# Kernel tuning notes

Measured on AMD Instinct MI355X. Metric: run time of the kernel, lower is better.

The kernel has to match this reference:

```python
import jax, jax.numpy as jnp
import numpy as np

N = 50000       # nodes
E = 800000      # edges (before self-loops)
IN_DIM = 128
HID = 64
HEADS = 4
C = HID // HEADS  # 16 per-head channels
NEG_SLOPE = 0.2   # PyG GATConv default
BN_EPS = 1e-5


def setup_inputs() -> dict:
    key = jax.random.key(0)
    ks = jax.random.split(key, 16)
    inp = {
        "x": jax.random.normal(ks[0], (N, IN_DIM), jnp.float32),
        "edge_index": jax.random.randint(ks[1], (2, E), 0, N, dtype=jnp.int32),
    }
    def glorot(k, shape):
        fan = sum(shape)
        return jax.random.normal(k, shape, jnp.float32) * jnp.sqrt(2.0 / fan)
    # layer 0: in=IN_DIM, layer 1: in=HID
    inp["W0"] = glorot(ks[2], (IN_DIM, HEADS * C))
    inp["a_src0"] = glorot(ks[3], (HEADS, C))
    inp["a_dst0"] = glorot(ks[4], (HEADS, C))
    inp["b0"] = jnp.zeros((HEADS * C,), jnp.float32)
    inp["g0"] = jnp.ones((HID,), jnp.float32)
    inp["be0"] = jnp.zeros((HID,), jnp.float32)
    inp["W1"] = glorot(ks[5], (HID, HEADS * C))
    inp["a_src1"] = glorot(ks[6], (HEADS, C))
    inp["a_dst1"] = glorot(ks[7], (HEADS, C))
    inp["b1"] = jnp.zeros((HEADS * C,), jnp.float32)
    inp["g1"] = jnp.ones((HID,), jnp.float32)
    inp["be1"] = jnp.zeros((HID,), jnp.float32)
    return inp


def _segment_softmax(e, dst, n):
    # softmax over edges grouped by destination node, per head. e: [Et, H]
    m = jax.ops.segment_max(e, dst, num_segments=n)          # [N, H]
    ex = jnp.exp(e - m[dst])
    s = jax.ops.segment_sum(ex, dst, num_segments=n)         # [N, H]
    return ex / (s[dst] + 1e-16)


def _gat_conv(h, src, dst, W, a_s, a_d, b):
    n = h.shape[0]
    hp = (h @ W).reshape(n, HEADS, C)                        # [N, H, C]
    al_s = jnp.einsum('nhc,hc->nh', hp, a_s)                 # [N, H]
    al_d = jnp.einsum('nhc,hc->nh', hp, a_d)
    e = jax.nn.leaky_relu(al_s[src] + al_d[dst], NEG_SLOPE)  # [Et, H]
    alpha = _segment_softmax(e, dst, n)
    msg = hp[src] * alpha[:, :, None]                        # [Et, H, C]
    out = jax.ops.segment_sum(msg, dst, num_segments=n)      # [N, H, C]
    return out.reshape(n, HEADS * C) + b


def _batch_norm(h, g, b):
    mu = h.mean(axis=0)
    var = h.var(axis=0)
    return (h - mu) * jax.lax.rsqrt(var + BN_EPS) * g + b


def reference(x, edge_index, W0, a_src0, a_dst0, b0, g0, be0,
              W1, a_src1, a_dst1, b1, g1, be1):
    n = x.shape[0]
    loops = jnp.arange(n, dtype=edge_index.dtype)
    src = jnp.concatenate([edge_index[0], loops])  # PyG adds self-loops
    dst = jnp.concatenate([edge_index[1], loops])
    h = _gat_conv(x, src, dst, W0, a_src0, a_dst0, b0)
    h = _batch_norm(h, g0, be0)
    h = jax.nn.relu(h)  # dropout: identity (eval / deterministic)
    h = _gat_conv(h, src, dst, W1, a_src1, a_dst1, b1)
    h = _batch_norm(h, g1, be1)
    return h
```

## Files before the change

kernel.cpp:

```cpp
#include <hip/hip_runtime.h>
#include <hip/hip_fp16.h>

#define CAP 128

__device__ __forceinline__ float sel4(float4 v, int h) {
  return h == 0 ? v.x : h == 1 ? v.y : h == 2 ? v.z : v.w;
}

template<int K, bool APPLY_BN>
__global__ void __launch_bounds__(256, 4)
gemm_tiled(const float* __restrict__ X, const float* __restrict__ W,
           const float* __restrict__ a_s, const float* __restrict__ a_d,
           const float* __restrict__ bnsum, const float* __restrict__ bnsq,
           const float* __restrict__ g, const float* __restrict__ be,
           __half* __restrict__ hp, float* __restrict__ al_s,
           float* __restrict__ al_d, int n)
{
  __shared__ float Wl[(K / 4) * 64 * 4];
  __shared__ float Xt[64 * K];

  for (int gi = threadIdx.x; gi < (K / 4) * 64; gi += 256) {
    int k4 = gi >> 6, ln = gi & 63;
    float4 w;
    w.x = W[(k4 * 4 + 0) * 64 + ln];
    w.y = W[(k4 * 4 + 1) * 64 + ln];
    w.z = W[(k4 * 4 + 2) * 64 + ln];
    w.w = W[(k4 * 4 + 3) * 64 + ln];
    *(float4*)&Wl[gi * 4] = w;
  }

  int row0 = blockIdx.x * 64;
  int nrows = min(64, n - row0);
  float4 sc, sh;
  if (APPLY_BN) {
    int cg = (threadIdx.x & 15) * 4;
    float inv_n = 1.f / (float)n;
#pragma unroll
    for (int q = 0; q < 4; ++q) {
      float mu  = bnsum[cg + q] * inv_n;
      float var = bnsq[cg + q] * inv_n - mu * mu;
      float s   = g[cg + q] * rsqrtf(var + 1e-5f);
      ((float*)&sc)[q] = s;
      ((float*)&sh)[q] = be[cg + q] - mu * s;
    }
  }
  const float4* src = (const float4*)(X + (size_t)row0 * K);
  int nf4 = nrows * (K / 4);
  for (int i = threadIdx.x; i < nf4; i += 256) {
    float4 v = src[i];
    if (APPLY_BN) {
      v.x = fmaxf(v.x * sc.x + sh.x, 0.f);
      v.y = fmaxf(v.y * sc.y + sh.y, 0.f);
      v.z = fmaxf(v.z * sc.z + sh.z, 0.f);
      v.w = fmaxf(v.w * sc.w + sh.w, 0.f);
    }
    *(float4*)&Xt[i * 4] = v;
  }
  __syncthreads();

  int lane = threadIdx.x & 63;
  int wid  = threadIdx.x >> 6;
  int rbase = wid * 16;
  float acc[16];
#pragma unroll
  for (int r = 0; r < 16; ++r) acc[r] = 0.f;

  for (int k4 = 0; k4 < K / 4; ++k4) {
    float4 wv = *(const float4*)&Wl[(k4 * 64 + lane) * 4];
#pragma unroll
    for (int r = 0; r < 16; ++r) {
      float4 xv = *(const float4*)&Xt[(rbase + r) * K + k4 * 4];
      acc[r] += xv.x * wv.x + xv.y * wv.y + xv.z * wv.z + xv.w * wv.w;
    }
  }

  float as_l = a_s[lane], ad_l = a_d[lane];
  int h = lane >> 4, c = lane & 15;
#pragma unroll
  for (int r = 0; r < 16; ++r) {
    int lr = rbase + r;
    if (lr >= nrows) break;
    int row = row0 + lr;
    float a = acc[r];
    hp[(size_t)row * 64 + lane] = __float2half(a);
    float vs = a * as_l;
    float vd = a * ad_l;
#pragma unroll
    for (int off = 8; off >= 1; off >>= 1) {
      vs += __shfl_xor(vs, off, 64);
      vd += __shfl_xor(vd, off, 64);
    }
    if (c == 0) { al_s[row * 4 + h] = vs; al_d[row * 4 + h] = vd; }
  }
}

__global__ void hist_k(const int* __restrict__ ei, int E, int N, int* __restrict__ count)
{
  int e = blockIdx.x * 256 + threadIdx.x;
  int Et = E + N;
  if (e >= Et) return;
  int d = (e < E) ? ei[E + e] : (e - E);
  atomicAdd(&count[d], 1);
}

__global__ void scan_block_k(const int* __restrict__ count, int* __restrict__ row_ptr,
                             int* __restrict__ partial, int n)
{
  __shared__ int woff[16];
  int tid = threadIdx.x;
  int i = blockIdx.x * 1024 + tid;
  int v = (i < n) ? count[i] : 0;
  int lane = tid & 63, wid = tid >> 6;
  int incl = v;
#pragma unroll
  for (int off = 1; off < 64; off <<= 1) {
    int t = __shfl_up(incl, off, 64);
    if (lane >= off) incl += t;
  }
  if (lane == 63) woff[wid] = incl;
  __syncthreads();
  if (tid < 16) {
    int wv = woff[tid];
    int winc = wv;
#pragma unroll
    for (int off = 1; off < 16; off <<= 1) {
      int t = __shfl_up(winc, off, 64);
      if (tid >= off) winc += t;
    }
    woff[tid] = winc - wv;
    if (tid == 15) partial[blockIdx.x] = winc;
  }
  __syncthreads();
  if (i < n) row_ptr[i] = woff[wid] + incl - v;
}

__global__ void scan_partial_k(int* __restrict__ partial, int* __restrict__ row_ptr,
                               int nb, int n)
{
  int tid = threadIdx.x;
  int v = (tid < nb) ? partial[tid] : 0;
  int incl = v;
#pragma unroll
  for (int off = 1; off < 64; off <<= 1) {
    int t = __shfl_up(incl, off, 64);
    if (tid >= off) incl += t;
  }
  if (tid < nb) partial[tid] = incl - v;
  if (tid == 63) row_ptr[n] = incl;
}

__global__ void scan_add_k(int* __restrict__ row_ptr, int* __restrict__ cursor,
                           const int* __restrict__ partial, int n)
{
  int i = blockIdx.x * 1024 + threadIdx.x;
  if (i < n) {
    int r = row_ptr[i] + partial[blockIdx.x];
    row_ptr[i] = r;
    cursor[i] = r;
  }
}

__global__ void scatter_k(const int* __restrict__ ei, int E, int N,
                          int* __restrict__ cursor, int* __restrict__ col_src)
{
  int e = blockIdx.x * 256 + threadIdx.x;
  int Et = E + N;
  if (e >= Et) return;
  int s, d;
  if (e < E) { s = ei[e]; d = ei[E + e]; } else { s = d = e - E; }
  int pos = atomicAdd(&cursor[d], 1);
  col_src[pos] = s;
}

__global__ void __launch_bounds__(256)
node_agg(const int* __restrict__ row_ptr, const int* __restrict__ col_src,
         const float* __restrict__ al_s, const float* __restrict__ al_d,
         const __half* __restrict__ hp, const float* __restrict__ bias,
         float* __restrict__ hpre, float* __restrict__ bnsum, float* __restrict__ bnsq,
         int n)
{
  __shared__ int   sh_s[4][CAP];
  __shared__ float sh_w[4][CAP * 4];
  __shared__ float sh_o[4][64];
  __shared__ float shs[64], shq[64];

  int lane = threadIdx.x & 63;
  int wid  = threadIdx.x >> 6;
  int c    = lane & 31;
  int e2   = lane >> 5;
  int h4   = c >> 3;
  float b  = bias[lane];
  float lsum = 0.f, lsq = 0.f;
  int nwaves = gridDim.x * 4;

  for (int d = blockIdx.x * 4 + wid; d < n; d += nwaves) {
    int beg = row_ptr[d], end = row_ptr[d + 1];
    int deg = end - beg;
    float4 ald4 = *(const float4*)(al_d + (size_t)d * 4);
    float p0 = 0.f, p1 = 0.f, p2 = 0.f, p3 = 0.f;
    float acc0 = 0.f, acc1 = 0.f;

    if (deg <= CAP) {
      int degR = (deg + 15) & ~15;
      for (int jb = 0; jb < degR; jb += 64) {
        int jj = jb + lane;
        if (jj < deg) {
          int s = __builtin_nontemporal_load(&col_src[beg + jj]);
          float4 a = *(const float4*)(al_s + (size_t)s * 4);
          float ex = a.x + ald4.x; ex = ex >= 0.f ? ex : 0.2f * ex;
          float ey = a.y + ald4.y; ey = ey >= 0.f ? ey : 0.2f * ey;
          float ez = a.z + ald4.z; ez = ez >= 0.f ? ez : 0.2f * ez;
          float ew = a.w + ald4.w; ew = ew >= 0.f ? ew : 0.2f * ew;
          ex = __expf(ex); ey = __expf(ey); ez = __expf(ez); ew = __expf(ew);
          sh_s[wid][jj] = s;
          *(float4*)&sh_w[wid][jj * 4] = make_float4(ex, ey, ez, ew);
          p0 += ex; p1 += ey; p2 += ez; p3 += ew;
        } else if (jj < degR) {
          sh_s[wid][jj] = 0;
          *(float4*)&sh_w[wid][jj * 4] = make_float4(0.f, 0.f, 0.f, 0.f);
        }
      }
#pragma unroll
      for (int off = 32; off >= 1; off >>= 1) {
        p0 += __shfl_xor(p0, off, 64);
        p1 += __shfl_xor(p1, off, 64);
        p2 += __shfl_xor(p2, off, 64);
        p3 += __shfl_xor(p3, off, 64);
      }
      __builtin_amdgcn_wave_barrier();
      for (int j = 0; j < degR; j += 16) {
#pragma unroll
        for (int k = 0; k < 8; ++k) {
          int e = j + k * 2 + e2;
          int s = sh_s[wid][e];
          float wh = sh_w[wid][e * 4 + h4];
          unsigned raw = *(const unsigned*)(hp + (size_t)s * 64 + c * 2);
          float2 f = __half22float2(*(const __half2*)&raw);
          acc0 += wh * f.x;
          acc1 += wh * f.y;
        }
      }
      acc0 += __shfl_xor(acc0, 32, 64);
      acc1 += __shfl_xor(acc1, 32, 64);
    } else {
      for (int j = beg; j < end; ++j) {
        int s = col_src[j];
        float4 a = *(const float4*)(al_s + (size_t)s * 4);
        float ex = a.x + ald4.x; ex = ex >= 0.f ? ex : 0.2f * ex;
        float ey = a.y + ald4.y; ey = ey >= 0.f ? ey : 0.2f * ey;
        float ez = a.z + ald4.z; ez = ez >= 0.f ? ez : 0.2f * ez;
        float ew = a.w + ald4.w; ew = ew >= 0.f ? ew : 0.2f * ew;
        ex = __expf(ex); ey = __expf(ey); ez = __expf(ez); ew = __expf(ew);
        p0 += ex; p1 += ey; p2 += ez; p3 += ew;
        float4 w4 = make_float4(ex, ey, ez, ew);
        float wh = sel4(w4, h4);
        unsigned raw = *(const unsigned*)(hp + (size_t)s * 64 + c * 2);
        float2 f = __half22float2(*(const __half2*)&raw);
        acc0 += wh * f.x;
        acc1 += wh * f.y;
      }
    }

    if (lane < 32) *(float2*)&sh_o[wid][c * 2] = make_float2(acc0, acc1);
    __builtin_amdgcn_wave_barrier();
    float den = (lane < 16) ? p0 : (lane < 32) ? p1 : (lane < 48) ? p2 : p3;
    float outv = sh_o[wid][lane] / (den + 1e-16f) + b;

    __builtin_nontemporal_store(outv, &hpre[(size_t)d * 64 + lane]);
    lsum += outv; lsq += outv * outv;
  }

  if (threadIdx.x < 64) { shs[threadIdx.x] = 0.f; shq[threadIdx.x] = 0.f; }
  __syncthreads();
  atomicAdd(&shs[lane], lsum);
  atomicAdd(&shq[lane], lsq);
  __syncthreads();
  if (threadIdx.x < 64) {
    atomicAdd(&bnsum[threadIdx.x], shs[threadIdx.x]);
    atomicAdd(&bnsq[threadIdx.x],  shq[threadIdx.x]);
  }
}

__global__ void bn_apply(float* __restrict__ buf, const float* __restrict__ bnsum,
                         const float* __restrict__ bnsq, const float* __restrict__ g,
                         const float* __restrict__ be, int n)
{
  size_t i = (size_t)blockIdx.x * 256 + threadIdx.x;
  size_t total = (size_t)n * 64;
  if (i >= total) return;
  int c = (int)(i & 63);
  float inv_n = 1.f / (float)n;
  float mu  = bnsum[c] * inv_n;
  float var = bnsq[c] * inv_n - mu * mu;
  buf[i] = (buf[i] - mu) * rsqrtf(var + 1e-5f) * g[c] + be[c];
}

extern "C" void kernel_launch(void* const* d_in, const int* in_sizes, int n_in,
                              void* d_out, int out_size, void* d_ws, size_t ws_size,
                              hipStream_t stream) {
  const float* x   = (const float*)d_in[0];
  const int*   ei  = (const int*)d_in[1];
  const float* W0  = (const float*)d_in[2];
  const float* as0 = (const float*)d_in[3];
  const float* ad0 = (const float*)d_in[4];
  const float* b0  = (const float*)d_in[5];
  const float* g0  = (const float*)d_in[6];
  const float* be0 = (const float*)d_in[7];
  const float* W1  = (const float*)d_in[8];
  const float* as1 = (const float*)d_in[9];
  const float* ad1 = (const float*)d_in[10];
  const float* b1  = (const float*)d_in[11];
  const float* g1  = (const float*)d_in[12];
  const float* be1 = (const float*)d_in[13];
  float* out = (float*)d_out;

  int N = in_sizes[0] / 128;
  int E = in_sizes[1] / 2;
  int Et = E + N;

  char* w = (char*)d_ws;
  auto alloc = [&](size_t bytes) {
    char* p = w; w += (bytes + 255) & ~255ull; return p;
  };
  int*    count = (int*)alloc((size_t)N * 4 + 4 * 64 * 4);
  float*  bnsum0 = (float*)(count + N);
  float*  bnsq0  = bnsum0 + 64;
  float*  bnsum1 = bnsq0 + 64;
  float*  bnsq1  = bnsum1 + 64;
  __half* hp    = (__half*)alloc((size_t)N * 64 * 2);
  float*  hpre0 = (float*)alloc((size_t)N * 64 * 4);
  float*  als   = (float*)alloc((size_t)N * 4 * 4);
  float*  ald   = (float*)alloc((size_t)N * 4 * 4);
  int*    rowp  = (int*)alloc((size_t)(N + 1) * 4);
  int*    cursor= (int*)alloc((size_t)N * 4);
  int*    parts = (int*)alloc(64 * 4);
  int*    csrc  = (int*)alloc((size_t)Et * 4);

  dim3 blk(256);
  int gEt   = (Et + 255) / 256;
  int gN64  = (N * 64 + 255) / 256;
  int nb    = (N + 1023) / 1024;
  int gTile = (N + 63) / 64;

  hipMemsetAsync(count, 0, (size_t)N * 4 + 4 * 64 * 4, stream);

  hist_k<<<gEt, blk, 0, stream>>>(ei, E, N, count);
  scan_block_k<<<nb, 1024, 0, stream>>>(count, rowp, parts, N);
  scan_partial_k<<<1, 64, 0, stream>>>(parts, rowp, nb, N);
  scan_add_k<<<nb, 1024, 0, stream>>>(rowp, cursor, parts, N);
  scatter_k<<<gEt, blk, 0, stream>>>(ei, E, N, cursor, csrc);

  gemm_tiled<128, false><<<gTile, blk, 0, stream>>>(x, W0, as0, ad0,
                                                    nullptr, nullptr, nullptr, nullptr,
                                                    hp, als, ald, N);
  node_agg<<<2048, blk, 0, stream>>>(rowp, csrc, als, ald, hp, b0,
                                     hpre0, bnsum0, bnsq0, N);

  gemm_tiled<64, true><<<gTile, blk, 0, stream>>>(hpre0, W1, as1, ad1,
                                                  bnsum0, bnsq0, g0, be0,
                                                  hp, als, ald, N);
  node_agg<<<2048, blk, 0, stream>>>(rowp, csrc, als, ald, hp, b1,
                                     out, bnsum1, bnsq1, N);
  bn_apply<<<gN64, blk, 0, stream>>>(out, bnsum1, bnsq1, g1, be1, N);
}
```

Measured before the change: 325.8 us.

## Fold partial scan into last block and single-pass small-degree aggregation

Removes the separate partial-scan kernel launch by having the last-finishing block of the block scan (detected via an atomic done counter) scan the partials. In node aggregation, lowers the small-degree cap to 64 so each lane handles at most one edge in a single pass, pads to multiples of 2 instead of 16, and adds a tail loop. The CAP change routes higher-degree nodes to the slower serial path, which is rare for this random graph (average degree about 17).

```diff
diff --git a/kernel.cpp b/kernel.cpp
--- a/kernel.cpp
+++ b/kernel.cpp
@@ -1,7 +1,7 @@
 #include <hip/hip_runtime.h>
 #include <hip/hip_fp16.h>
 
-#define CAP 128
+#define CAP 64
 
 __device__ __forceinline__ float sel4(float4 v, int h) {
   return h == 0 ? v.x : h == 1 ? v.y : h == 2 ? v.z : v.w;
@@ -104,9 +104,11 @@
 }
 
 __global__ void scan_block_k(const int* __restrict__ count, int* __restrict__ row_ptr,
-                             int* __restrict__ partial, int n)
+                             int* __restrict__ partial, int* __restrict__ done_ctr,
+                             int nb, int n)
 {
   __shared__ int woff[16];
+  __shared__ int is_last;
   int tid = threadIdx.x;
   int i = blockIdx.x * 1024 + tid;
   int v = (i < n) ? count[i] : 0;
@@ -132,21 +134,22 @@
   }
   __syncthreads();
   if (i < n) row_ptr[i] = woff[wid] + incl - v;
-}
-
-__global__ void scan_partial_k(int* __restrict__ partial, int* __restrict__ row_ptr,
-                               int nb, int n)
-{
-  int tid = threadIdx.x;
-  int v = (tid < nb) ? partial[tid] : 0;
-  int incl = v;
-#pragma unroll
-  for (int off = 1; off < 64; off <<= 1) {
-    int t = __shfl_up(incl, off, 64);
-    if (tid >= off) incl += t;
-  }
-  if (tid < nb) partial[tid] = incl - v;
-  if (tid == 63) row_ptr[n] = incl;
+
+  __threadfence();
+  if (tid == 0) is_last = (atomicAdd(done_ctr, 1) == nb - 1) ? 1 : 0;
+  __syncthreads();
+  if (is_last && tid < 64) {
+    int pv = (tid < nb) ? partial[tid] : 0;
+    int pincl = pv;
+#pragma unroll
+    for (int off = 1; off < 64; off <<= 1) {
+      int t = __shfl_up(pincl, off, 64);
+      if (tid >= off) pincl += t;
+    }
+    if (tid < nb) partial[tid] = pincl - pv;
+    if (tid == 63) row_ptr[n] = pincl;
+    __threadfence();
+  }
 }
 
 __global__ void scan_add_k(int* __restrict__ row_ptr, int* __restrict__ cursor,
@@ -199,36 +202,29 @@
     float4 ald4 = *(const float4*)(al_d + (size_t)d * 4);
     float p0 = 0.f, p1 = 0.f, p2 = 0.f, p3 = 0.f;
     float acc0 = 0.f, acc1 = 0.f;
+    float outv;
 
     if (deg <= CAP) {
-      int degR = (deg + 15) & ~15;
-      for (int jb = 0; jb < degR; jb += 64) {
-        int jj = jb + lane;
-        if (jj < deg) {
-          int s = __builtin_nontemporal_load(&col_src[beg + jj]);
-          float4 a = *(const float4*)(al_s + (size_t)s * 4);
-          float ex = a.x + ald4.x; ex = ex >= 0.f ? ex : 0.2f * ex;
-          float ey = a.y + ald4.y; ey = ey >= 0.f ? ey : 0.2f * ey;
-          float ez = a.z + ald4.z; ez = ez >= 0.f ? ez : 0.2f * ez;
-          float ew = a.w + ald4.w; ew = ew >= 0.f ? ew : 0.2f * ew;
-          ex = __expf(ex); ey = __expf(ey); ez = __expf(ez); ew = __expf(ew);
-          sh_s[wid][jj] = s;
-          *(float4*)&sh_w[wid][jj * 4] = make_float4(ex, ey, ez, ew);
-          p0 += ex; p1 += ey; p2 += ez; p3 += ew;
-        } else if (jj < degR) {
-          sh_s[wid][jj] = 0;
-          *(float4*)&sh_w[wid][jj * 4] = make_float4(0.f, 0.f, 0.f, 0.f);
-        }
-      }
-#pragma unroll
-      for (int off = 32; off >= 1; off >>= 1) {
-        p0 += __shfl_xor(p0, off, 64);
-        p1 += __shfl_xor(p1, off, 64);
-        p2 += __shfl_xor(p2, off, 64);
-        p3 += __shfl_xor(p3, off, 64);
+      int degR = (deg + 1) & ~1;
+      if (lane < deg) {
+        int s = __builtin_nontemporal_load(&col_src[beg + lane]);
+        float4 a = *(const float4*)(al_s + (size_t)s * 4);
+        float ex = a.x + ald4.x; ex = ex >= 0.f ? ex : 0.2f * ex;
+        float ey = a.y + ald4.y; ey = ey >= 0.f ? ey : 0.2f * ey;
+        float ez = a.z + ald4.z; ez = ez >= 0.f ? ez : 0.2f * ez;
+        float ew = a.w + ald4.w; ew = ew >= 0.f ? ew : 0.2f * ew;
+        ex = __expf(ex); ey = __expf(ey); ez = __expf(ez); ew = __expf(ew);
+        sh_s[wid][lane] = s;
+        *(float4*)&sh_w[wid][lane * 4] = make_float4(ex, ey, ez, ew);
+        p0 = ex; p1 = ey; p2 = ez; p3 = ew;
+      } else if (lane < degR) {
+        sh_s[wid][lane] = 0;
+        *(float4*)&sh_w[wid][lane * 4] = make_float4(0.f, 0.f, 0.f, 0.f);
       }
       __builtin_amdgcn_wave_barrier();
-      for (int j = 0; j < degR; j += 16) {
+
+      int j = 0;
+      for (; j + 16 <= degR; j += 16) {
 #pragma unroll
         for (int k = 0; k < 8; ++k) {
           int e = j + k * 2 + e2;
@@ -240,8 +236,30 @@
           acc1 += wh * f.y;
         }
       }
+      for (; j < degR; j += 2) {
+        int e = j + e2;
+        int s = sh_s[wid][e];
+        float wh = sh_w[wid][e * 4 + h4];
+        unsigned raw = *(const unsigned*)(hp + (size_t)s * 64 + c * 2);
+        float2 f = __half22float2(*(const __half2*)&raw);
+        acc0 += wh * f.x;
+        acc1 += wh * f.y;
+      }
       acc0 += __shfl_xor(acc0, 32, 64);
       acc1 += __shfl_xor(acc1, 32, 64);
+
+#pragma unroll
+      for (int off = 32; off >= 1; off >>= 1) {
+        p0 += __shfl_xor(p0, off, 64);
+        p1 += __shfl_xor(p1, off, 64);
+        p2 += __shfl_xor(p2, off, 64);
+        p3 += __shfl_xor(p3, off, 64);
+      }
+
+      if (lane < 32) *(float2*)&sh_o[wid][c * 2] = make_float2(acc0, acc1);
+      __builtin_amdgcn_wave_barrier();
+      float den = (lane < 16) ? p0 : (lane < 32) ? p1 : (lane < 48) ? p2 : p3;
+      outv = sh_o[wid][lane] / (den + 1e-16f) + b;
     } else {
       for (int j = beg; j < end; ++j) {
         int s = col_src[j];
@@ -252,19 +270,19 @@
         float ew = a.w + ald4.w; ew = ew >= 0.f ? ew : 0.2f * ew;
         ex = __expf(ex); ey = __expf(ey); ez = __expf(ez); ew = __expf(ew);
         p0 += ex; p1 += ey; p2 += ez; p3 += ew;
-        float4 w4 = make_float4(ex, ey, ez, ew);
-        float wh = sel4(w4, h4);
+        float wh = sel4(make_float4(ex, ey, ez, ew), h4);
         unsigned raw = *(const unsigned*)(hp + (size_t)s * 64 + c * 2);
         float2 f = __half22float2(*(const __half2*)&raw);
         acc0 += wh * f.x;
         acc1 += wh * f.y;
       }
-    }
-
-    if (lane < 32) *(float2*)&sh_o[wid][c * 2] = make_float2(acc0, acc1);
-    __builtin_amdgcn_wave_barrier();
-    float den = (lane < 16) ? p0 : (lane < 32) ? p1 : (lane < 48) ? p2 : p3;
-    float outv = sh_o[wid][lane] / (den + 1e-16f) + b;
+      acc0 += __shfl_xor(acc0, 32, 64);
+      acc1 += __shfl_xor(acc1, 32, 64);
+      if (lane < 32) *(float2*)&sh_o[wid][c * 2] = make_float2(acc0, acc1);
+      __builtin_amdgcn_wave_barrier();
+      float den = (lane < 16) ? p0 : (lane < 32) ? p1 : (lane < 48) ? p2 : p3;
+      outv = sh_o[wid][lane] / (den + 1e-16f) + b;
+    }
 
     __builtin_nontemporal_store(outv, &hpre[(size_t)d * 64 + lane]);
     lsum += outv; lsq += outv * outv;
@@ -322,11 +340,12 @@
   auto alloc = [&](size_t bytes) {
     char* p = w; w += (bytes + 255) & ~255ull; return p;
   };
-  int*    count = (int*)alloc((size_t)N * 4 + 4 * 64 * 4);
+  int*    count = (int*)alloc((size_t)N * 4 + 4 * 64 * 4 + 4);
   float*  bnsum0 = (float*)(count + N);
   float*  bnsq0  = bnsum0 + 64;
   float*  bnsum1 = bnsq0 + 64;
   float*  bnsq1  = bnsum1 + 64;
+  int*    done_ctr = (int*)(bnsq1 + 64);
   __half* hp    = (__half*)alloc((size_t)N * 64 * 2);
   float*  hpre0 = (float*)alloc((size_t)N * 64 * 4);
   float*  als   = (float*)alloc((size_t)N * 4 * 4);
@@ -342,11 +361,10 @@
   int nb    = (N + 1023) / 1024;
   int gTile = (N + 63) / 64;
 
-  hipMemsetAsync(count, 0, (size_t)N * 4 + 4 * 64 * 4, stream);
+  hipMemsetAsync(count, 0, (size_t)N * 4 + 4 * 64 * 4 + 4, stream);
 
   hist_k<<<gEt, blk, 0, stream>>>(ei, E, N, count);
-  scan_block_k<<<nb, 1024, 0, stream>>>(count, rowp, parts, N);
-  scan_partial_k<<<1, 64, 0, stream>>>(parts, rowp, nb, N);
+  scan_block_k<<<nb, 1024, 0, stream>>>(count, rowp, parts, done_ctr, nb, N);
   scan_add_k<<<nb, 1024, 0, stream>>>(rowp, cursor, parts, N);
   scatter_k<<<gEt, blk, 0, stream>>>(ei, E, N, cursor, csrc);
 
```

Result: slower. 359.9 us (+10.5%).
